# Kernel optimization log

Measured on AMD Instinct MI355X. Metric: run time of the kernel, lower is better.

Reference implementation:

```python
import jax, jax.numpy as jnp
import numpy as np

N_ROIS = 2000
FH, FW, C = 50, 50, 512
PH, PW = 7, 7
N_CLASS = 21
IMG = 800
FC_IN = PH * PW * C  # 25088
FC_OUT = 4096


def crop_and_resize(img, boxes, ph, pw):
    """Faithful jax port of tf.image.crop_and_resize (bilinear, extrapolation 0).
    img: [H, W, C]; boxes: [N, 4] normalized (y1, x1, y2, x2). Returns [N, ph, pw, C]."""
    H, W, _ = img.shape
    y1, x1, y2, x2 = boxes[:, 0], boxes[:, 1], boxes[:, 2], boxes[:, 3]
    iy = jnp.arange(ph, dtype=boxes.dtype)
    ix = jnp.arange(pw, dtype=boxes.dtype)
    # TF sampling grid: in_y = y1*(H-1) + i * (y2-y1)*(H-1)/(crop_h-1)
    in_y = y1[:, None] * (H - 1) + iy[None, :] * ((y2 - y1)[:, None] * (H - 1) / (ph - 1))  # [N, ph]
    in_x = x1[:, None] * (W - 1) + ix[None, :] * ((x2 - x1)[:, None] * (W - 1) / (pw - 1))  # [N, pw]
    y0f = jnp.floor(in_y); x0f = jnp.floor(in_x)
    ylerp = (in_y - y0f)[:, :, None, None]   # [N, ph, 1, 1]
    xlerp = (in_x - x0f)[:, None, :, None]   # [N, 1, pw, 1]
    y0 = jnp.clip(y0f, 0, H - 1).astype(jnp.int32)
    y1i = jnp.clip(y0f + 1, 0, H - 1).astype(jnp.int32)
    x0 = jnp.clip(x0f, 0, W - 1).astype(jnp.int32)
    x1i = jnp.clip(x0f + 1, 0, W - 1).astype(jnp.int32)

    def gather(yi, xi):  # [N,ph],[N,pw] -> [N,ph,pw,C]
        return img[yi[:, :, None], xi[:, None, :]]

    top = gather(y0, x0) * (1 - xlerp) + gather(y0, x1i) * xlerp
    bot = gather(y1i, x0) * (1 - xlerp) + gather(y1i, x1i) * xlerp
    out = top * (1 - ylerp) + bot * ylerp
    valid = ((in_y >= 0) & (in_y <= H - 1))[:, :, None] & ((in_x >= 0) & (in_x <= W - 1))[:, None, :]
    return jnp.where(valid[..., None], out, jnp.zeros((), out.dtype))


def setup_inputs() -> dict:
    key = jax.random.key(0)
    kf, ky, kx, k1, k2, k3, k4, k5, k6 = jax.random.split(key, 9)
    feature = jax.random.normal(kf, (1, FH, FW, C), dtype=jnp.float32)
    # valid boxes in original-image coordinates: y1<y2, x1<x2 within [0, IMG]
    ys = jnp.sort(jax.random.uniform(ky, (N_ROIS, 2), dtype=jnp.float32) * IMG, axis=1)
    xs = jnp.sort(jax.random.uniform(kx, (N_ROIS, 2), dtype=jnp.float32) * IMG, axis=1)
    rois = jnp.stack([ys[:, 0], xs[:, 0], ys[:, 1], xs[:, 1]], axis=1)
    W_fc = jax.random.normal(k1, (FC_IN, FC_OUT), dtype=jnp.float32) * 0.01
    b_fc = jnp.zeros((FC_OUT,), dtype=jnp.float32)
    W_loc = jax.random.normal(k3, (FC_OUT, N_CLASS * 4), dtype=jnp.float32) * 0.01
    b_loc = jnp.zeros((N_CLASS * 4,), dtype=jnp.float32)
    W_score = jax.random.normal(k5, (FC_OUT, N_CLASS), dtype=jnp.float32) * 0.01
    b_score = jnp.zeros((N_CLASS,), dtype=jnp.float32)
    return {"feature": feature, "rois": rois, "img_h": IMG, "img_w": IMG,
            "W_fc": W_fc, "b_fc": b_fc, "W_loc": W_loc, "b_loc": b_loc,
            "W_score": W_score, "b_score": b_score}


def reference(feature, rois, img_h, img_w, W_fc, b_fc, W_loc, b_loc, W_score, b_score):
    norm = jnp.array([img_h, img_w, img_h, img_w], dtype=jnp.float32)
    boxes = rois / norm                      # normalized [y1,x1,y2,x2]
    pool = crop_and_resize(feature[0], boxes, PH, PW)  # [N, 7, 7, 512]
    flat = pool.reshape(rois.shape[0], -1)   # [N, 25088]
    fc = flat @ W_fc + b_fc                  # [N, 4096]
    roi_cls_locs = fc @ W_loc + b_loc        # [N, 84]
    roi_scores = fc @ W_score + b_score      # [N, 21]
    return roi_cls_locs, roi_scores
```

## Files before the change

kernel.cpp:

```cpp
#include <hip/hip_runtime.h>
#include <stdint.h>


typedef float          f32x4 __attribute__((ext_vector_type(4)));
typedef __bf16         bfx8  __attribute__((ext_vector_type(8)));
typedef __bf16         bfx4  __attribute__((ext_vector_type(4)));
typedef __bf16         bfx2  __attribute__((ext_vector_type(2)));

#define KBIG 25088
#define NMID 4096
#define NROIS 2000
#define G1BLOCKS 784
#define SPLITS 28

__device__ __forceinline__ void gll16(const void* g, void* l) {
  __builtin_amdgcn_global_load_lds(
      (const __attribute__((address_space(1))) void*)(uintptr_t)(g),
      (__attribute__((address_space(3))) void*)(uintptr_t)(l), 16, 0, 0);
}

__global__ __launch_bounds__(256) void k_prep(const float* __restrict__ Wl,
                                              const float* __restrict__ Ws,
                                              const float* __restrict__ bfc,
                                              const float* __restrict__ bl,
                                              const float* __restrict__ bs,
                                              unsigned short* __restrict__ WcatT,
                                              float* __restrict__ bc) {
  if (blockIdx.x < 2048) {
    int idx = blockIdx.x * 256 + threadIdx.x;
    int c = idx >> 12, k = idx & 4095;
    float v = 0.0f;
    if (c < 84)       v = Wl[k * 84 + c];
    else if (c < 105) v = Ws[k * 21 + (c - 84)];
    ((__bf16*)WcatT)[idx] = (__bf16)v;
  } else {
    int c = blockIdx.x - 2048;
    int t = threadIdx.x;
    __shared__ float red[256];
    float p = 0.0f;
    if (c < 105) {
      for (int k = t; k < 4096; k += 256) {
        float w = (c < 84) ? Wl[k * 84 + c] : Ws[k * 21 + (c - 84)];
        p += bfc[k] * w;
      }
    }
    red[t] = p;
    __syncthreads();
    for (int s = 128; s > 0; s >>= 1) {
      if (t < s) red[t] += red[t + s];
      __syncthreads();
    }
    if (t == 0) {
      float bias = (c < 84) ? bl[c] : (c < 105 ? bs[c - 84] : 0.0f);
      bc[c] = (c < 105) ? (red[0] + bias) : 0.0f;
    }
  }
}

__global__ __launch_bounds__(256, 2) void k_pool_gemm1(
    const float* __restrict__ F, const float* __restrict__ rois,
    const int* __restrict__ ihp, const int* __restrict__ iwp,
    unsigned short* __restrict__ A,
    const float* __restrict__ Wfc, const unsigned short* __restrict__ WcatT,
    float* __restrict__ Pg1) {
  const int t = threadIdx.x;
  __shared__ __align__(16) char sA[32768];
  __shared__ __align__(16) char sB[32768];
  if (blockIdx.x < G1BLOCKS) {
    const int lane = t & 63, wid = t >> 6;
    const int wm = wid >> 1, wn = wid & 1;
    const int l15 = lane & 15, l4 = lane >> 4;
    const int mt = blockIdx.x >> 1, sp = blockIdx.x & 1;
    const int m0 = mt * 64;
    const int kbase = sp * 2048;
    const int rot = mt & 31;
    const int jlog = (t & 7) ^ ((t >> 3) & 7);
    f32x4 acc[2][4] = {};

    const float* abase = Wfc + (size_t)m0 * NMID + kbase;
    const int arow_lo = lane >> 4;
    const int aswz = lane & 15;

    auto rc = [&](int c) { return (c + rot) & 31; };

    auto stageA = [&](int c, int off) {
      const int k0 = rc(c) * 64;
#pragma unroll
      for (int q = 0; q < 4; ++q) {
        const int o = wid * 4 + q;
        const int r = o * 4 + arow_lo;
        const int clog = aswz ^ (r & 15);
        gll16(abase + (size_t)r * NMID + k0 + clog * 4, sA + off + o * 1024);
      }
    };
    auto stageB = [&](int c, int off) {
      const int k0 = rc(c) * 64;
#pragma unroll
      for (int q = 0; q < 4; ++q)
        gll16(WcatT + (size_t)(q * 32 + (t >> 3)) * NMID + kbase + k0 + jlog * 8,
              sB + off + q * 4096 + wid * 1024);
    };
    auto compute = [&](int aoff, int boff) {
#pragma unroll
      for (int kk = 0; kk < 2; ++kk) {
        bfx8 af[2];
#pragma unroll
        for (int mi = 0; mi < 2; ++mi) {
          const int R = wm * 32 + mi * 16 + l15;
          const int cb = kk * 8 + l4 * 2;
          f32x4 a0 = *(const f32x4*)(sA + aoff + R * 256 + (((cb + 0) ^ (R & 15)) << 4));
          f32x4 a1 = *(const f32x4*)(sA + aoff + R * 256 + (((cb + 1) ^ (R & 15)) << 4));
          bfx8 tb;
#pragma unroll
          for (int j = 0; j < 4; ++j) {
            tb[j] = (__bf16)a0[j];
            tb[j + 4] = (__bf16)a1[j];
          }
          af[mi] = tb;
        }
        bfx8 bfr[4];
#pragma unroll
        for (int ni = 0; ni < 4; ++ni) {
          const int row = wn * 64 + ni * 16 + l15;
          bfr[ni] = *(const bfx8*)(sB + boff + row * 128 + ((((kk << 2) + l4) ^ (row & 7)) << 4));
        }
#pragma unroll
        for (int mi = 0; mi < 2; ++mi)
#pragma unroll
          for (int ni = 0; ni < 4; ++ni)
            acc[mi][ni] = __builtin_amdgcn_mfma_f32_16x16x32_bf16(af[mi], bfr[ni], acc[mi][ni], 0, 0, 0);
      }
    };

    stageA(0, 0);
    stageB(0, 0);
    for (int cc = 0; cc < 16; ++cc) {
      const int c0 = cc * 2;
      stageA(c0 + 1, 16384);
      stageB(c0 + 1, 16384);
      asm volatile("s_waitcnt vmcnt(8)" ::: "memory");
      __builtin_amdgcn_s_barrier();
      __builtin_amdgcn_sched_barrier(0);
      compute(0, 0);
      __builtin_amdgcn_s_barrier();
      const int cn = (c0 + 2 < 32) ? c0 + 2 : 31;
      stageA(cn, 0);
      stageB(cn, 0);
      asm volatile("s_waitcnt vmcnt(8)" ::: "memory");
      __builtin_amdgcn_s_barrier();
      __builtin_amdgcn_sched_barrier(0);
      compute(16384, 16384);
      __builtin_amdgcn_s_barrier();
    }
    asm volatile("s_waitcnt vmcnt(0)" ::: "memory");
#pragma unroll
    for (int mi = 0; mi < 2; ++mi)
#pragma unroll
      for (int ni = 0; ni < 4; ++ni) {
        const int n = wn * 64 + ni * 16 + l15;
        float* dst = Pg1 + ((size_t)sp * 128 + n) * KBIG + m0 + wm * 32 + mi * 16 + l4 * 4;
        *(f32x4*)dst = acc[mi][ni];
      }
  } else {
    const int r = blockIdx.x - G1BLOCKS;
    const float ih = (float)ihp[0], iw = (float)iwp[0];
    const float y1 = rois[r * 4 + 0] / ih;
    const float x1 = rois[r * 4 + 1] / iw;
    const float y2 = rois[r * 4 + 2] / ih;
    const float x2 = rois[r * 4 + 3] / iw;
    const float sy = (y2 - y1) * 49.0f / 6.0f;
    const float sx = (x2 - x1) * 49.0f / 6.0f;
    const int ch = t * 2;
    __bf16* __restrict__ Arow = (__bf16*)(A + (size_t)r * KBIG);

    auto cellcoords = [&](int cell, int& o00, int& o01, int& o10, int& o11,
                          float& yl, float& xl, bool& valid) {
      const int iy = cell / 7, ix = cell - iy * 7;
      const float in_y = y1 * 49.0f + (float)iy * sy;
      const float in_x = x1 * 49.0f + (float)ix * sx;
      const float y0f = floorf(in_y), x0f = floorf(in_x);
      yl = in_y - y0f; xl = in_x - x0f;
      const int y0  = (int)fminf(fmaxf(y0f, 0.0f), 49.0f);
      const int y1i = (int)fminf(fmaxf(y0f + 1.0f, 0.0f), 49.0f);
      const int x0  = (int)fminf(fmaxf(x0f, 0.0f), 49.0f);
      const int x1i = (int)fminf(fmaxf(x0f + 1.0f, 0.0f), 49.0f);
      valid = (in_y >= 0.0f) && (in_y <= 49.0f) && (in_x >= 0.0f) && (in_x <= 49.0f);
      o00 = (y0 * 50 + x0) * 512;  o01 = (y0 * 50 + x1i) * 512;
      o10 = (y1i * 50 + x0) * 512; o11 = (y1i * 50 + x1i) * 512;
    };

    int o00, o01, o10, o11; float yl, xl; bool valid;
    cellcoords(0, o00, o01, o10, o11, yl, xl, valid);
    float2 f00 = *(const float2*)&F[o00 + ch];
    float2 f01 = *(const float2*)&F[o01 + ch];
    float2 f10 = *(const float2*)&F[o10 + ch];
    float2 f11 = *(const float2*)&F[o11 + ch];

    for (int cell = 0; cell < 49; ++cell) {
      const float2 g00 = f00, g01 = f01, g10 = f10, g11 = f11;
      const float pyl = yl, pxl = xl;
      const bool pv = valid;
      if (cell < 48) {
        cellcoords(cell + 1, o00, o01, o10, o11, yl, xl, valid);
        f00 = *(const float2*)&F[o00 + ch];
        f01 = *(const float2*)&F[o01 + ch];
        f10 = *(const float2*)&F[o10 + ch];
        f11 = *(const float2*)&F[o11 + ch];
      }
      float oA = 0.0f, oB = 0.0f;
      if (pv) {
        float t0 = g00.x * (1.0f - pxl) + g01.x * pxl;
        float t1 = g00.y * (1.0f - pxl) + g01.y * pxl;
        float b0 = g10.x * (1.0f - pxl) + g11.x * pxl;
        float b1 = g10.y * (1.0f - pxl) + g11.y * pxl;
        oA = t0 * (1.0f - pyl) + b0 * pyl;
        oB = t1 * (1.0f - pyl) + b1 * pyl;
      }
      bfx2 v; v[0] = (__bf16)oA; v[1] = (__bf16)oB;
      *(bfx2*)(Arow + cell * 512 + ch) = v;
    }
  }
}

__global__ __launch_bounds__(256) void k_addcvt(const float* __restrict__ Pg1,
                                                unsigned short* __restrict__ WcT) {
  const size_t i = ((size_t)blockIdx.x * 256 + threadIdx.x) * 8;
  f32x4 a0 = *(const f32x4*)(Pg1 + i);
  f32x4 a1 = *(const f32x4*)(Pg1 + i + 4);
  f32x4 b0 = *(const f32x4*)(Pg1 + 3211264 + i);
  f32x4 b1 = *(const f32x4*)(Pg1 + 3211264 + i + 4);
  bfx8 o;
#pragma unroll
  for (int j = 0; j < 4; ++j) {
    o[j]     = (__bf16)(a0[j] + b0[j]);
    o[j + 4] = (__bf16)(a1[j] + b1[j]);
  }
  *(bfx8*)(WcT + i) = o;
}

__global__ __launch_bounds__(256) void k_gemm2(const unsigned short* __restrict__ Ap,
                                               const unsigned short* __restrict__ WcT,
                                               float* __restrict__ P) {
  __shared__ __align__(16) char S[49152];
  const int t = threadIdx.x;
  const int lane = t & 63, wid = t >> 6;
  const int wm = wid >> 1, wn = wid & 1;
  const int l15 = lane & 15, l4 = lane >> 4;
  const int mt = blockIdx.x, sp = blockIdx.y;
  const int kbase = sp * 896;
  const int jlog = (t & 7) ^ ((t >> 3) & 7);
  f32x4 acc[2][4] = {};

  int ar0 = mt * 64 + (t >> 3);
  int ar1 = ar0 + 32;
  if (ar0 > NROIS - 1) ar0 = NROIS - 1;
  if (ar1 > NROIS - 1) ar1 = NROIS - 1;
  const unsigned short* asrc0 = Ap + (size_t)ar0 * KBIG + jlog * 8;
  const unsigned short* asrc1 = Ap + (size_t)ar1 * KBIG + jlog * 8;

  auto stage2 = [&](int c, int off) {
    const int k0 = kbase + c * 64;
    gll16(asrc0 + k0, S + off + wid * 1024);
    gll16(asrc1 + k0, S + off + 4096 + wid * 1024);
#pragma unroll
    for (int q = 0; q < 4; ++q)
      gll16(WcT + (size_t)(q * 32 + (t >> 3)) * KBIG + k0 + jlog * 8,
            S + off + 8192 + q * 4096 + wid * 1024);
  };
  auto compute2 = [&](int off) {
#pragma unroll
    for (int kh = 0; kh < 2; ++kh) {
      bfx8 af[2], bfr[4];
#pragma unroll
      for (int mi = 0; mi < 2; ++mi) {
        const int row = wm * 32 + mi * 16 + l15;
        af[mi] = *(const bfx8*)(S + off + row * 128 + ((((kh << 2) + l4) ^ (row & 7)) << 4));
      }
#pragma unroll
      for (int ni = 0; ni < 4; ++ni) {
        const int row = wn * 64 + ni * 16 + l15;
        bfr[ni] = *(const bfx8*)(S + off + 8192 + row * 128 + ((((kh << 2) + l4) ^ (row & 7)) << 4));
      }
#pragma unroll
      for (int mi = 0; mi < 2; ++mi)
#pragma unroll
        for (int ni = 0; ni < 4; ++ni)
          acc[mi][ni] = __builtin_amdgcn_mfma_f32_16x16x32_bf16(af[mi], bfr[ni], acc[mi][ni], 0, 0, 0);
    }
  };

  stage2(0, 0);
  for (int cc = 0; cc < 7; ++cc) {
    const int c0 = cc * 2;
    stage2(c0 + 1, 24576);
    asm volatile("s_waitcnt vmcnt(6)" ::: "memory");
    __builtin_amdgcn_s_barrier();
    __builtin_amdgcn_sched_barrier(0);
    compute2(0);
    __builtin_amdgcn_s_barrier();
    stage2((c0 + 2 < 14) ? c0 + 2 : 13, 0);
    asm volatile("s_waitcnt vmcnt(6)" ::: "memory");
    __builtin_amdgcn_s_barrier();
    __builtin_amdgcn_sched_barrier(0);
    compute2(24576);
    __builtin_amdgcn_s_barrier();
  }
  asm volatile("s_waitcnt vmcnt(0)" ::: "memory");
  float* out = P + (size_t)(mt * SPLITS + sp) * 8192;
#pragma unroll
  for (int mi = 0; mi < 2; ++mi)
#pragma unroll
    for (int ni = 0; ni < 4; ++ni)
#pragma unroll
      for (int i = 0; i < 4; ++i)
        out[(wm * 32 + mi * 16 + l4 * 4 + i) * 128 + wn * 64 + ni * 16 + l15] = acc[mi][ni][i];
}

__global__ __launch_bounds__(128) void k_reduce(const float* __restrict__ P,
                                                const float* __restrict__ bc,
                                                float* __restrict__ out) {
  const int m = blockIdx.x;
  const int c = threadIdx.x;
  if (c >= 105) return;
  const int mt = m >> 6, r = m & 63;
  float sum = 0.0f;
#pragma unroll
  for (int s = 0; s < SPLITS; ++s)
    sum += P[(size_t)(mt * SPLITS + s) * 8192 + r * 128 + c];
  sum += bc[c];
  if (c < 84) out[m * 84 + c] = sum;
  else        out[168000 + m * 21 + (c - 84)] = sum;
}

extern "C" void kernel_launch(void* const* d_in, const int* in_sizes, int n_in,
                              void* d_out, int out_size, void* d_ws, size_t ws_size,
                              hipStream_t stream) {
  const float* F    = (const float*)d_in[0];
  const float* rois = (const float*)d_in[1];
  const int*   ih   = (const int*)d_in[2];
  const int*   iw   = (const int*)d_in[3];
  const float* Wfc  = (const float*)d_in[4];
  const float* bfc  = (const float*)d_in[5];
  const float* Wl   = (const float*)d_in[6];
  const float* bl   = (const float*)d_in[7];
  const float* Ws   = (const float*)d_in[8];
  const float* bs   = (const float*)d_in[9];
  (void)in_sizes; (void)n_in; (void)out_size; (void)ws_size;

  char* ws = (char*)d_ws;
  unsigned short* Apool = (unsigned short*)(ws);
  unsigned short* WcatT = (unsigned short*)(ws + 100352000);
  unsigned short* WcT   = (unsigned short*)(ws + 101400576);
  float*          bc    = (float*)(ws + 107823104);
  float*          P     = (float*)(ws + 107823616);
  float*          Pg1   = (float*)(ws + 137183744);
  float*          out   = (float*)d_out;

  k_prep      <<<2176, 256, 0, stream>>>(Wl, Ws, bfc, bl, bs, WcatT, bc);
  k_pool_gemm1<<<G1BLOCKS + NROIS, 256, 0, stream>>>(F, rois, ih, iw, Apool,
                                                     Wfc, WcatT, Pg1);
  k_addcvt    <<<1568, 256, 0, stream>>>(Pg1, WcT);
  k_gemm2     <<<dim3(32, SPLITS), 256, 0, stream>>>(Apool, WcT, P);
  k_reduce    <<<NROIS, 128, 0, stream>>>(P, bc, out);
}
```

Baseline: 236.6 us.

## Pre-convert W_fc to bf16 and split pooling out of the fused gemm1 kernel

Adds a separate pass that converts the fp32 W_fc weight matrix to bf16. The gemm1 kernel then loads bf16 A tiles directly, with no per-fragment fp32-to-bf16 conversion in the inner loop and half the LDS traffic for A. The crop-and-resize pooling, which shared one launch with gemm1, now runs as its own kernel. The cost is an extra full read of the 400 MB fp32 weight plus a 200 MB bf16 write each call, and the pooling no longer overlaps with gemm1.

```diff
diff --git a/kernel.cpp b/kernel.cpp
--- a/kernel.cpp
+++ b/kernel.cpp
@@ -4,14 +4,13 @@
 
 typedef float          f32x4 __attribute__((ext_vector_type(4)));
 typedef __bf16         bfx8  __attribute__((ext_vector_type(8)));
-typedef __bf16         bfx4  __attribute__((ext_vector_type(4)));
 typedef __bf16         bfx2  __attribute__((ext_vector_type(2)));
 
 #define KBIG 25088
 #define NMID 4096
 #define NROIS 2000
-#define G1BLOCKS 784
 #define SPLITS 28
+#define PG1STRIDE 3211264
 
 __device__ __forceinline__ void gll16(const void* g, void* l) {
   __builtin_amdgcn_global_load_lds(
@@ -57,169 +56,111 @@
   }
 }
 
-__global__ __launch_bounds__(256, 2) void k_pool_gemm1(
-    const float* __restrict__ F, const float* __restrict__ rois,
-    const int* __restrict__ ihp, const int* __restrict__ iwp,
-    unsigned short* __restrict__ A,
-    const float* __restrict__ Wfc, const unsigned short* __restrict__ WcatT,
-    float* __restrict__ Pg1) {
+__global__ __launch_bounds__(256) void k_cvt(const float* __restrict__ in,
+                                             unsigned short* __restrict__ outp) {
+  __bf16* out = (__bf16*)outp;
+  const size_t S = 3211264;
+  size_t i = ((size_t)blockIdx.x * 256 + threadIdx.x) * 8;
+#pragma unroll 1
+  for (int o = 0; o < 8; ++o) {
+    f32x4 a0 = *(const f32x4*)(in + i);
+    f32x4 a1 = *(const f32x4*)(in + i + 4);
+    f32x4 b0 = *(const f32x4*)(in + i + S);
+    f32x4 b1 = *(const f32x4*)(in + i + S + 4);
+    f32x4 c0 = *(const f32x4*)(in + i + 2 * S);
+    f32x4 c1 = *(const f32x4*)(in + i + 2 * S + 4);
+    f32x4 d0 = *(const f32x4*)(in + i + 3 * S);
+    f32x4 d1 = *(const f32x4*)(in + i + 3 * S + 4);
+    bfx8 oa, ob, oc, od;
+#pragma unroll
+    for (int j = 0; j < 4; ++j) {
+      oa[j] = (__bf16)a0[j]; oa[j + 4] = (__bf16)a1[j];
+      ob[j] = (__bf16)b0[j]; ob[j + 4] = (__bf16)b1[j];
+      oc[j] = (__bf16)c0[j]; oc[j + 4] = (__bf16)c1[j];
+      od[j] = (__bf16)d0[j]; od[j + 4] = (__bf16)d1[j];
+    }
+    *(bfx8*)(out + i)         = oa;
+    *(bfx8*)(out + i + S)     = ob;
+    *(bfx8*)(out + i + 2 * S) = oc;
+    *(bfx8*)(out + i + 3 * S) = od;
+    i += 4 * S;
+  }
+}
+
+__global__ __launch_bounds__(256) void k_gemm1b(const unsigned short* __restrict__ WfcB,
+                                                const unsigned short* __restrict__ WcatT,
+                                                float* __restrict__ Pg1) {
+  __shared__ __align__(16) char S[49152];
   const int t = threadIdx.x;
-  __shared__ __align__(16) char sA[32768];
-  __shared__ __align__(16) char sB[32768];
-  if (blockIdx.x < G1BLOCKS) {
-    const int lane = t & 63, wid = t >> 6;
-    const int wm = wid >> 1, wn = wid & 1;
-    const int l15 = lane & 15, l4 = lane >> 4;
-    const int mt = blockIdx.x >> 1, sp = blockIdx.x & 1;
-    const int m0 = mt * 64;
-    const int kbase = sp * 2048;
-    const int rot = mt & 31;
-    const int jlog = (t & 7) ^ ((t >> 3) & 7);
-    f32x4 acc[2][4] = {};
-
-    const float* abase = Wfc + (size_t)m0 * NMID + kbase;
-    const int arow_lo = lane >> 4;
-    const int aswz = lane & 15;
-
-    auto rc = [&](int c) { return (c + rot) & 31; };
-
-    auto stageA = [&](int c, int off) {
-      const int k0 = rc(c) * 64;
-#pragma unroll
-      for (int q = 0; q < 4; ++q) {
-        const int o = wid * 4 + q;
-        const int r = o * 4 + arow_lo;
-        const int clog = aswz ^ (r & 15);
-        gll16(abase + (size_t)r * NMID + k0 + clog * 4, sA + off + o * 1024);
-      }
-    };
-    auto stageB = [&](int c, int off) {
-      const int k0 = rc(c) * 64;
-#pragma unroll
-      for (int q = 0; q < 4; ++q)
-        gll16(WcatT + (size_t)(q * 32 + (t >> 3)) * NMID + kbase + k0 + jlog * 8,
-              sB + off + q * 4096 + wid * 1024);
-    };
-    auto compute = [&](int aoff, int boff) {
-#pragma unroll
-      for (int kk = 0; kk < 2; ++kk) {
-        bfx8 af[2];
-#pragma unroll
-        for (int mi = 0; mi < 2; ++mi) {
-          const int R = wm * 32 + mi * 16 + l15;
-          const int cb = kk * 8 + l4 * 2;
-          f32x4 a0 = *(const f32x4*)(sA + aoff + R * 256 + (((cb + 0) ^ (R & 15)) << 4));
-          f32x4 a1 = *(const f32x4*)(sA + aoff + R * 256 + (((cb + 1) ^ (R & 15)) << 4));
-          bfx8 tb;
-#pragma unroll
-          for (int j = 0; j < 4; ++j) {
-            tb[j] = (__bf16)a0[j];
-            tb[j + 4] = (__bf16)a1[j];
-          }
-          af[mi] = tb;
-        }
-        bfx8 bfr[4];
-#pragma unroll
-        for (int ni = 0; ni < 4; ++ni) {
-          const int row = wn * 64 + ni * 16 + l15;
-          bfr[ni] = *(const bfx8*)(sB + boff + row * 128 + ((((kk << 2) + l4) ^ (row & 7)) << 4));
-        }
-#pragma unroll
-        for (int mi = 0; mi < 2; ++mi)
-#pragma unroll
-          for (int ni = 0; ni < 4; ++ni)
-            acc[mi][ni] = __builtin_amdgcn_mfma_f32_16x16x32_bf16(af[mi], bfr[ni], acc[mi][ni], 0, 0, 0);
-      }
-    };
-
-    stageA(0, 0);
-    stageB(0, 0);
-    for (int cc = 0; cc < 16; ++cc) {
-      const int c0 = cc * 2;
-      stageA(c0 + 1, 16384);
-      stageB(c0 + 1, 16384);
-      asm volatile("s_waitcnt vmcnt(8)" ::: "memory");
-      __builtin_amdgcn_s_barrier();
-      __builtin_amdgcn_sched_barrier(0);
-      compute(0, 0);
-      __builtin_amdgcn_s_barrier();
-      const int cn = (c0 + 2 < 32) ? c0 + 2 : 31;
-      stageA(cn, 0);
-      stageB(cn, 0);
-      asm volatile("s_waitcnt vmcnt(8)" ::: "memory");
-      __builtin_amdgcn_s_barrier();
-      __builtin_amdgcn_sched_barrier(0);
-      compute(16384, 16384);
-      __builtin_amdgcn_s_barrier();
-    }
-    asm volatile("s_waitcnt vmcnt(0)" ::: "memory");
-#pragma unroll
-    for (int mi = 0; mi < 2; ++mi)
+  const int lane = t & 63, wid = t >> 6;
+  const int wm = wid >> 1, wn = wid & 1;
+  const int l15 = lane & 15, l4 = lane >> 4;
+  const int mt = blockIdx.x, sp = blockIdx.y;
+  const int m0 = mt * 64;
+  const int kbase = sp * 2048;
+  const int jlog = (t & 7) ^ ((t >> 3) & 7);
+  f32x4 acc[2][4] = {};
+
+  const unsigned short* asrc0 = WfcB + (size_t)(m0 + (t >> 3)) * NMID + jlog * 8;
+  const unsigned short* asrc1 = asrc0 + (size_t)32 * NMID;
+
+  auto stage2 = [&](int c, int off) {
+    const int k0 = kbase + c * 64;
+    gll16(asrc0 + k0, S + off + wid * 1024);
+    gll16(asrc1 + k0, S + off + 4096 + wid * 1024);
+#pragma unroll
+    for (int q = 0; q < 4; ++q)
+      gll16(WcatT + (size_t)(q * 32 + (t >> 3)) * NMID + k0 + jlog * 8,
+            S + off + 8192 + q * 4096 + wid * 1024);
+  };
+  auto compute2 = [&](int off) {
+#pragma unroll
+    for (int kh = 0; kh < 2; ++kh) {
+      bfx8 af[2], bfr[4];
+#pragma unroll
+      for (int mi = 0; mi < 2; ++mi) {
+        const int row = wm * 32 + mi * 16 + l15;
+        af[mi] = *(const bfx8*)(S + off + row * 128 + ((((kh << 2) + l4) ^ (row & 7)) << 4));
+      }
 #pragma unroll
       for (int ni = 0; ni < 4; ++ni) {
-        const int n = wn * 64 + ni * 16 + l15;
-        float* dst = Pg1 + ((size_t)sp * 128 + n) * KBIG + m0 + wm * 32 + mi * 16 + l4 * 4;
-        *(f32x4*)dst = acc[mi][ni];
-      }
-  } else {
-    const int r = blockIdx.x - G1BLOCKS;
-    const float ih = (float)ihp[0], iw = (float)iwp[0];
-    const float y1 = rois[r * 4 + 0] / ih;
-    const float x1 = rois[r * 4 + 1] / iw;
-    const float y2 = rois[r * 4 + 2] / ih;
-    const float x2 = rois[r * 4 + 3] / iw;
-    const float sy = (y2 - y1) * 49.0f / 6.0f;
-    const float sx = (x2 - x1) * 49.0f / 6.0f;
-    const int ch = t * 2;
-    __bf16* __restrict__ Arow = (__bf16*)(A + (size_t)r * KBIG);
-
-    auto cellcoords = [&](int cell, int& o00, int& o01, int& o10, int& o11,
-                          float& yl, float& xl, bool& valid) {
-      const int iy = cell / 7, ix = cell - iy * 7;
-      const float in_y = y1 * 49.0f + (float)iy * sy;
-      const float in_x = x1 * 49.0f + (float)ix * sx;
-      const float y0f = floorf(in_y), x0f = floorf(in_x);
-      yl = in_y - y0f; xl = in_x - x0f;
-      const int y0  = (int)fminf(fmaxf(y0f, 0.0f), 49.0f);
-      const int y1i = (int)fminf(fmaxf(y0f + 1.0f, 0.0f), 49.0f);
-      const int x0  = (int)fminf(fmaxf(x0f, 0.0f), 49.0f);
-      const int x1i = (int)fminf(fmaxf(x0f + 1.0f, 0.0f), 49.0f);
-      valid = (in_y >= 0.0f) && (in_y <= 49.0f) && (in_x >= 0.0f) && (in_x <= 49.0f);
-      o00 = (y0 * 50 + x0) * 512;  o01 = (y0 * 50 + x1i) * 512;
-      o10 = (y1i * 50 + x0) * 512; o11 = (y1i * 50 + x1i) * 512;
-    };
-
-    int o00, o01, o10, o11; float yl, xl; bool valid;
-    cellcoords(0, o00, o01, o10, o11, yl, xl, valid);
-    float2 f00 = *(const float2*)&F[o00 + ch];
-    float2 f01 = *(const float2*)&F[o01 + ch];
-    float2 f10 = *(const float2*)&F[o10 + ch];
-    float2 f11 = *(const float2*)&F[o11 + ch];
-
-    for (int cell = 0; cell < 49; ++cell) {
-      const float2 g00 = f00, g01 = f01, g10 = f10, g11 = f11;
-      const float pyl = yl, pxl = xl;
-      const bool pv = valid;
-      if (cell < 48) {
-        cellcoords(cell + 1, o00, o01, o10, o11, yl, xl, valid);
-        f00 = *(const float2*)&F[o00 + ch];
-        f01 = *(const float2*)&F[o01 + ch];
-        f10 = *(const float2*)&F[o10 + ch];
-        f11 = *(const float2*)&F[o11 + ch];
-      }
-      float oA = 0.0f, oB = 0.0f;
-      if (pv) {
-        float t0 = g00.x * (1.0f - pxl) + g01.x * pxl;
-        float t1 = g00.y * (1.0f - pxl) + g01.y * pxl;
-        float b0 = g10.x * (1.0f - pxl) + g11.x * pxl;
-        float b1 = g10.y * (1.0f - pxl) + g11.y * pxl;
-        oA = t0 * (1.0f - pyl) + b0 * pyl;
-        oB = t1 * (1.0f - pyl) + b1 * pyl;
-      }
-      bfx2 v; v[0] = (__bf16)oA; v[1] = (__bf16)oB;
-      *(bfx2*)(Arow + cell * 512 + ch) = v;
-    }
-  }
+        const int row = wn * 64 + ni * 16 + l15;
+        bfr[ni] = *(const bfx8*)(S + off + 8192 + row * 128 + ((((kh << 2) + l4) ^ (row & 7)) << 4));
+      }
+#pragma unroll
+      for (int mi = 0; mi < 2; ++mi)
+#pragma unroll
+        for (int ni = 0; ni < 4; ++ni)
+          acc[mi][ni] = __builtin_amdgcn_mfma_f32_16x16x32_bf16(af[mi], bfr[ni], acc[mi][ni], 0, 0, 0);
+    }
+  };
+
+  stage2(0, 0);
+  for (int cc = 0; cc < 16; ++cc) {
+    const int c0 = cc * 2;
+    stage2(c0 + 1, 24576);
+    asm volatile("s_waitcnt vmcnt(6)" ::: "memory");
+    __builtin_amdgcn_s_barrier();
+    __builtin_amdgcn_sched_barrier(0);
+    compute2(0);
+    __builtin_amdgcn_s_barrier();
+    stage2((c0 + 2 < 32) ? c0 + 2 : 31, 0);
+    asm volatile("s_waitcnt vmcnt(6)" ::: "memory");
+    __builtin_amdgcn_s_barrier();
+    __builtin_amdgcn_sched_barrier(0);
+    compute2(24576);
+    __builtin_amdgcn_s_barrier();
+  }
+  asm volatile("s_waitcnt vmcnt(0)" ::: "memory");
+  float* base = Pg1 + (size_t)sp * PG1STRIDE;
+#pragma unroll
+  for (int mi = 0; mi < 2; ++mi)
+#pragma unroll
+    for (int ni = 0; ni < 4; ++ni) {
+      const int n = wn * 64 + ni * 16 + l15;
+      const int m = m0 + wm * 32 + mi * 16 + l4 * 4;
+      *(f32x4*)(base + (size_t)n * KBIG + m) = acc[mi][ni];
+    }
 }
 
 __global__ __launch_bounds__(256) void k_addcvt(const float* __restrict__ Pg1,
@@ -227,8 +168,8 @@
   const size_t i = ((size_t)blockIdx.x * 256 + threadIdx.x) * 8;
   f32x4 a0 = *(const f32x4*)(Pg1 + i);
   f32x4 a1 = *(const f32x4*)(Pg1 + i + 4);
-  f32x4 b0 = *(const f32x4*)(Pg1 + 3211264 + i);
-  f32x4 b1 = *(const f32x4*)(Pg1 + 3211264 + i + 4);
+  f32x4 b0 = *(const f32x4*)(Pg1 + PG1STRIDE + i);
+  f32x4 b1 = *(const f32x4*)(Pg1 + PG1STRIDE + i + 4);
   bfx8 o;
 #pragma unroll
   for (int j = 0; j < 4; ++j) {
@@ -236,6 +177,71 @@
     o[j + 4] = (__bf16)(a1[j] + b1[j]);
   }
   *(bfx8*)(WcT + i) = o;
+}
+
+__global__ __launch_bounds__(256) void k_pool(const float* __restrict__ F,
+                                              const float* __restrict__ rois,
+                                              const int* __restrict__ ihp,
+                                              const int* __restrict__ iwp,
+                                              unsigned short* __restrict__ A) {
+  const int r = blockIdx.x;
+  const int t = threadIdx.x;
+  const float ih = (float)ihp[0], iw = (float)iwp[0];
+  const float y1 = rois[r * 4 + 0] / ih;
+  const float x1 = rois[r * 4 + 1] / iw;
+  const float y2 = rois[r * 4 + 2] / ih;
+  const float x2 = rois[r * 4 + 3] / iw;
+  const float sy = (y2 - y1) * 49.0f / 6.0f;
+  const float sx = (x2 - x1) * 49.0f / 6.0f;
+  const int ch = t * 2;
+  __bf16* __restrict__ Arow = (__bf16*)(A + (size_t)r * KBIG);
+
+  auto cellcoords = [&](int cell, int& o00, int& o01, int& o10, int& o11,
+                        float& yl, float& xl, bool& valid) {
+    const int iy = cell / 7, ix = cell - iy * 7;
+    const float in_y = y1 * 49.0f + (float)iy * sy;
+    const float in_x = x1 * 49.0f + (float)ix * sx;
+    const float y0f = floorf(in_y), x0f = floorf(in_x);
+    yl = in_y - y0f; xl = in_x - x0f;
+    const int y0  = (int)fminf(fmaxf(y0f, 0.0f), 49.0f);
+    const int y1i = (int)fminf(fmaxf(y0f + 1.0f, 0.0f), 49.0f);
+    const int x0  = (int)fminf(fmaxf(x0f, 0.0f), 49.0f);
+    const int x1i = (int)fminf(fmaxf(x0f + 1.0f, 0.0f), 49.0f);
+    valid = (in_y >= 0.0f) && (in_y <= 49.0f) && (in_x >= 0.0f) && (in_x <= 49.0f);
+    o00 = (y0 * 50 + x0) * 512;  o01 = (y0 * 50 + x1i) * 512;
+    o10 = (y1i * 50 + x0) * 512; o11 = (y1i * 50 + x1i) * 512;
+  };
+
+  int o00, o01, o10, o11; float yl, xl; bool valid;
+  cellcoords(0, o00, o01, o10, o11, yl, xl, valid);
+  float2 f00 = *(const float2*)&F[o00 + ch];
+  float2 f01 = *(const float2*)&F[o01 + ch];
+  float2 f10 = *(const float2*)&F[o10 + ch];
+  float2 f11 = *(const float2*)&F[o11 + ch];
+
+  for (int cell = 0; cell < 49; ++cell) {
+    const float2 g00 = f00, g01 = f01, g10 = f10, g11 = f11;
+    const float pyl = yl, pxl = xl;
+    const bool pv = valid;
+    if (cell < 48) {
+      cellcoords(cell + 1, o00, o01, o10, o11, yl, xl, valid);
+      f00 = *(const float2*)&F[o00 + ch];
+      f01 = *(const float2*)&F[o01 + ch];
+      f10 = *(const float2*)&F[o10 + ch];
+      f11 = *(const float2*)&F[o11 + ch];
+    }
+    float oA = 0.0f, oB = 0.0f;
+    if (pv) {
+      float t0 = g00.x * (1.0f - pxl) + g01.x * pxl;
+      float t1 = g00.y * (1.0f - pxl) + g01.y * pxl;
+      float b0 = g10.x * (1.0f - pxl) + g11.x * pxl;
+      float b1 = g10.y * (1.0f - pxl) + g11.y * pxl;
+      oA = t0 * (1.0f - pyl) + b0 * pyl;
+      oB = t1 * (1.0f - pyl) + b1 * pyl;
+    }
+    bfx2 v; v[0] = (__bf16)oA; v[1] = (__bf16)oB;
+    *(bfx2*)(Arow + cell * 512 + ch) = v;
+  }
 }
 
 __global__ __launch_bounds__(256) void k_gemm2(const unsigned short* __restrict__ Ap,
@@ -354,12 +360,14 @@
   float*          bc    = (float*)(ws + 107823104);
   float*          P     = (float*)(ws + 107823616);
   float*          Pg1   = (float*)(ws + 137183744);
+  unsigned short* WfcB  = (unsigned short*)(ws + 162873856);
   float*          out   = (float*)d_out;
 
-  k_prep      <<<2176, 256, 0, stream>>>(Wl, Ws, bfc, bl, bs, WcatT, bc);
-  k_pool_gemm1<<<G1BLOCKS + NROIS, 256, 0, stream>>>(F, rois, ih, iw, Apool,
-                                                     Wfc, WcatT, Pg1);
-  k_addcvt    <<<1568, 256, 0, stream>>>(Pg1, WcT);
-  k_gemm2     <<<dim3(32, SPLITS), 256, 0, stream>>>(Apool, WcT, P);
-  k_reduce    <<<NROIS, 128, 0, stream>>>(P, bc, out);
-}
+  k_prep  <<<2176, 256, 0, stream>>>(Wl, Ws, bfc, bl, bs, WcatT, bc);
+  k_cvt   <<<1568, 256, 0, stream>>>(Wfc, WfcB);
+  k_gemm1b<<<dim3(392, 2), 256, 0, stream>>>(WfcB, WcatT, Pg1);
+  k_addcvt<<<1568, 256, 0, stream>>>(Pg1, WcT);
+  k_pool  <<<NROIS, 256, 0, stream>>>(F, rois, ih, iw, Apool);
+  k_gemm2 <<<dim3(32, SPLITS), 256, 0, stream>>>(Apool, WcT, P);
+  k_reduce<<<NROIS, 128, 0, stream>>>(P, bc, out);
+}
```

Result: slower. 310.2 us (+31.1%).
